# Optimization experiments

Hardware: AMD Instinct MI355X
Metric: run time of the kernel (lower is better)

## Reference

```python
import jax, jax.numpy as jnp
import numpy as np
import math

B, T, D, H, DFF = 4, 1024, 1024, 16, 4096
HD = D // H

def _c(a):
    # a: float array [2, ...] -> complex64 (a[0] real, a[1] imag)
    return jax.lax.complex(a[0], a[1])

def _clinear(z, W, b):
    # complex y = z @ W^T + b (torch nn.Linear convention)
    return z @ _c(W).T + _c(b)

def _cln(z, g, b, eps=1e-5):
    # per-component LayerNorm with separate affine for real/imag parts
    def ln(r):
        m = r.mean(-1, keepdims=True)
        v = ((r - m) ** 2).mean(-1, keepdims=True)
        return (r - m) / jnp.sqrt(v + eps)
    return jax.lax.complex(ln(z.real) * g[0] + b[0], ln(z.imag) * g[1] + b[1])

def _rope_phasor(t_len, dim):
    inv_freq = 1.0 / (10000.0 ** (jnp.arange(dim, dtype=jnp.float32) / dim))
    freqs = jnp.arange(t_len, dtype=jnp.float32)[:, None] * inv_freq[None, :]
    return jax.lax.complex(jnp.cos(freqs), jnp.sin(freqs))  # [T, HD]


def setup_inputs():
    key = jax.random.key(0)
    ks = iter(jax.random.split(key, 40))
    def p(shape, scale=0.02):
        return jax.random.normal(next(ks), shape, jnp.float32) * scale
    inp = {"x": p((2, B, T, D), 1.0), "mask": jnp.tril(jnp.ones((T, T), bool))}
    dims = {"wq": (D, D), "wk": (D, D), "wv": (D, D), "wo": (D, D),
            "wf1": (DFF, D), "wf2": (D, DFF), "wg": (D, D)}
    for name, (o, i) in dims.items():
        inp[name] = p((2, o, i))
        inp["b" + name[1:]] = p((2, o))
    inp["g1"] = jnp.ones((2, D), jnp.float32)
    inp["b1"] = jnp.zeros((2, D), jnp.float32)
    inp["g2"] = jnp.ones((2, D), jnp.float32)
    inp["b2"] = jnp.zeros((2, D), jnp.float32)
    return inp


def reference(x, mask, wq, bq, wk, bk, wv, bv, wo, bo,
              wf1, bf1, wf2, bf2, wg, bg, g1, b1, g2, b2):
    z = _c(x)  # [B,T,D] complex64
    ph = _rope_phasor(T, HD)[None, None]  # [1,1,T,HD]

    # ---- attention branch (pre-norm) ----
    nz = _cln(z, g1, b1)
    heads = lambda t: t.reshape(B, T, H, HD).transpose(0, 2, 1, 3)  # [B,H,T,HD]
    q = heads(_clinear(nz, wq, bq)) * ph
    k = heads(_clinear(nz, wk, bk)) * ph
    v = heads(_clinear(nz, wv, bv))
    score = jnp.einsum('bhqd,bhkd->bhqk', q, jnp.conj(k)) / math.sqrt(HD)
    mag = jnp.where(mask, jnp.abs(score), jnp.float32(-1e9))
    aw = jax.nn.softmax(mag, axis=-1)
    awc = jax.lax.complex(aw, jnp.zeros_like(aw))
    o = jnp.einsum('bhqk,bhkd->bhqd', awc, v)
    o = o.transpose(0, 2, 1, 3).reshape(B, T, D)
    z = z + _clinear(o, wo, bo)

    # ---- FFN branch with CReLU and AntiMatterGate ----
    nz = _cln(z, g2, b2)
    h = _clinear(nz, wf1, bf1)
    h = jax.lax.complex(jax.nn.relu(h.real), jax.nn.relu(h.imag))  # CReLU
    h = _clinear(h, wf2, bf2)
    g = _clinear(h, wg, bg)
    gn = jnp.abs(g) + 1e-8
    h = h * (g / jax.lax.complex(gn, jnp.zeros_like(gn)))  # phase-only gate
    z = z + h
    return jnp.stack([z.real, z.imag], axis=0)  # [2,B,T,D] float32
```

## Files before the change

kernel.cpp:

```cpp
#include <hip/hip_runtime.h>
#include <math.h>

#define B_ 4
#define T_ 1024
#define D_ 1024
#define H_ 16
#define DFF_ 4096
#define HD_ 64
#define BT_ (B_*T_)
#define PL ((size_t)BT_*D_)

typedef unsigned int uint;
typedef unsigned short ushort;
typedef __attribute__((ext_vector_type(8))) __bf16 bf16x8;
typedef __attribute__((ext_vector_type(4))) float f32x4;
typedef __attribute__((ext_vector_type(4))) uint uint4v;

__device__ __forceinline__ float b2f(ushort u){
  union{uint i; float f;} x; x.i = ((uint)u)<<16; return x.f;
}
__device__ __forceinline__ ushort f2b(float f){
  union{float f; uint i;} x; x.f = f;
  uint r = x.i + 0x7fffu + ((x.i>>16)&1u);
  return (ushort)(r>>16);
}
__device__ __forceinline__ void fsplit(float x, ushort& hi, ushort& lo){
  hi = f2b(x);
  lo = f2b(x - b2f(hi));
}
__device__ __forceinline__ bf16x8 negv(bf16x8 v){
  union{bf16x8 b; uint4v u;} t; t.b = v;
  t.u ^= 0x80008000u;
  return t.b;
}
__device__ __forceinline__ f32x4 mfma16(bf16x8 a, bf16x8 b, f32x4 c){
  return __builtin_amdgcn_mfma_f32_16x16x32_bf16(a,b,c,0,0,0);
}
__device__ __forceinline__ float block_sum(float v, float* sm){
  #pragma unroll
  for (int o=32;o>0;o>>=1) v += __shfl_down(v,o);
  int wid = threadIdx.x>>6;
  if ((threadIdx.x&63)==0) sm[wid]=v;
  __syncthreads();
  float r = sm[0]+sm[1]+sm[2]+sm[3];
  __syncthreads();
  return r;
}

__global__ __launch_bounds__(256) void cvt_split(const float* __restrict__ s,
                                                 ushort* __restrict__ d, long NK){
  long i = ((long)blockIdx.x*256 + threadIdx.x)*4;
  if (i >= NK) return;
  float4 vr = *(const float4*)(s+i);
  float4 vi = *(const float4*)(s+NK+i);
  ushort4 rh, rl, ih4, il4;
  fsplit(vr.x, rh.x, rl.x); fsplit(vr.y, rh.y, rl.y);
  fsplit(vr.z, rh.z, rl.z); fsplit(vr.w, rh.w, rl.w);
  fsplit(vi.x, ih4.x, il4.x); fsplit(vi.y, ih4.y, il4.y);
  fsplit(vi.z, ih4.z, il4.z); fsplit(vi.w, ih4.w, il4.w);
  *(ushort4*)(d + i)        = rh;
  *(ushort4*)(d + NK + i)   = rl;
  *(ushort4*)(d + 2*NK + i) = ih4;
  *(ushort4*)(d + 3*NK + i) = il4;
}

__global__ __launch_bounds__(256) void cln_kernel(const float* __restrict__ x,
    long PSx, int row0, const float* __restrict__ g, const float* __restrict__ bb,
    ushort* __restrict__ out, long PSo)
{
  __shared__ float sm[4];
  int row = blockIdx.x, comp = blockIdx.y;
  const float* xr = x + (size_t)comp*PSx + (size_t)(row0+row)*D_;
  float4 v = *(const float4*)(xr + threadIdx.x*4);
  float s = v.x+v.y+v.z+v.w;
  s = block_sum(s, sm);
  float mean = s * (1.0f/D_);
  float dx=v.x-mean, dy=v.y-mean, dz=v.z-mean, dw=v.w-mean;
  float s2 = dx*dx+dy*dy+dz*dz+dw*dw;
  s2 = block_sum(s2, sm);
  float inv = 1.0f/sqrtf(s2*(1.0f/D_) + 1e-5f);
  float4 gv = *(const float4*)(g + comp*D_ + threadIdx.x*4);
  float4 bv = *(const float4*)(bb + comp*D_ + threadIdx.x*4);
  float y0 = dx*inv*gv.x + bv.x, y1 = dy*inv*gv.y + bv.y;
  float y2 = dz*inv*gv.z + bv.z, y3 = dw*inv*gv.w + bv.w;
  ushort4 hh, ll;
  fsplit(y0, hh.x, ll.x); fsplit(y1, hh.y, ll.y);
  fsplit(y2, hh.z, ll.z); fsplit(y3, hh.w, ll.w);
  ushort* oh = out + (size_t)(comp*2)*PSo   + (size_t)row*D_;
  ushort* ol = out + (size_t)(comp*2+1)*PSo + (size_t)row*D_;
  *(ushort4*)(oh + threadIdx.x*4) = hh;
  *(ushort4*)(ol + threadIdx.x*4) = ll;
}

template<int BM,int BN,int WM,int WN>
__global__ __launch_bounds__(256,1) void cgemm_split(
    const ushort* __restrict__ A, long PSa,
    const ushort* __restrict__ W, long PSw, long wstride,
    const float* b0, const float* b1, const float* b2,
    const float* __restrict__ Rr, const float* __restrict__ Ri,
    float* __restrict__ Cf, long PSc, long ostrideF,
    ushort* __restrict__ Cs, long PSs, long ostrideS,
    int M, int N, int K, int relu, int biasRow, int kslice)
{
  constexpr int NI = WM/16, NJ = WN/16;
  constexpr int NWX = BN/WN;
  constexpr int NPW = (BM+BN)/16;
  constexpr int BUF = (BM+BN)*128;
  __shared__ __align__(16) ushort lds[2*BUF];
  const int tid = threadIdx.x, wave = tid>>6, lane = tid&63;
  const int quad = lane>>4, l16 = lane&15;
  const int lrow = lane>>3, sl = lane&7;

  const int gx = gridDim.x, gy = gridDim.y;
  const int nt = gx*gy;
  int lin = blockIdx.x + gx*blockIdx.y;
  int tile = (nt&7) ? lin : ((lin&7)*(nt>>3) + (lin>>3));
  int bxi, byi;
  if (gx <= gy){ bxi = tile % gx; byi = tile / gx; }
  else         { byi = tile % gy; bxi = tile / gy; }
  const int bm = byi*BM, bn = bxi*BN;

  const int gz = blockIdx.z;
  W += (size_t)gz*wstride;
  const float* bias = (gz==0)? b0 : (gz==1)? b1 : b2;
  if (Cf) Cf += (size_t)gz*ostrideF;
  if (Cs) Cs += (size_t)gz*ostrideS;
  const int wm = (wave/NWX)*WM, wn = (wave%NWX)*WN;
  const int kbeg = kslice ? gz*kslice : 0;
  const int kend = kslice ? kbeg+kslice : K;

  int sa[4];
  #pragma unroll
  for (int p=0;p<4;p++) sa[p] = (((p&1)<<2) + quad) ^ (l16&7);

  auto STAGE = [&](int cur, int k0){
    #pragma unroll
    for (int n=0;n<NPW;n++){
      int it = wave*NPW + n;
      const ushort* mat; long PS; int brow, pair, r0, lbase;
      if (it < BM/4){
        pair = it/(BM/8); r0 = (it%(BM/8))*8;
        mat = A; PS = PSa; brow = bm;
        lbase = (pair*BM + r0)*8;
      } else {
        int itb = it - BM/4;
        pair = itb/(BN/8); r0 = (itb%(BN/8))*8;
        mat = W; PS = PSw; brow = bn;
        lbase = (2*BM + pair*BN + r0)*8;
      }
      int row = r0 + lrow;
      int s = sl ^ (row&7);
      int plane = pair*2 + (s>>2);
      const ushort* gp = mat + (size_t)plane*PS + (size_t)(brow+row)*K + k0 + (s&3)*8;
      __builtin_amdgcn_global_load_lds(
          (const __attribute__((address_space(1))) void*)gp,
          (__attribute__((address_space(3))) void*)&lds[cur*BUF + lbase*8], 16, 0, 0);
    }
  };

  f32x4 accr[NI][NJ], acci[NI][NJ];
  #pragma unroll
  for (int i=0;i<NI;i++)
    #pragma unroll
    for (int j=0;j<NJ;j++){
      accr[i][j] = (f32x4){0.f,0.f,0.f,0.f};
      acci[i][j] = (f32x4){0.f,0.f,0.f,0.f};
    }

  int cur = 0;
  STAGE(0, kbeg);
  for (int k0=kbeg; k0<kend; k0+=32){
    __syncthreads();
    if (k0+32 < kend) STAGE(cur^1, k0+32);
    const int cb = cur*BUF;

    bf16x8 Bf[NJ][4];
    #pragma unroll
    for (int j=0;j<NJ;j++){
      int row = wn + j*16 + l16;
      #pragma unroll
      for (int p=0;p<4;p++)
        Bf[j][p] = *(const bf16x8*)&lds[cb + BM*128 + ((p>>1)*BN + row)*64 + sa[p]*8];
    }
    #pragma unroll
    for (int i=0;i<NI;i++){
      int row = wm + i*16 + l16;
      bf16x8 A0 = *(const bf16x8*)&lds[cb + (0*BM + row)*64 + sa[0]*8];
      bf16x8 A1 = *(const bf16x8*)&lds[cb + (0*BM + row)*64 + sa[1]*8];
      bf16x8 A2 = *(const bf16x8*)&lds[cb + (1*BM + row)*64 + sa[2]*8];
      bf16x8 A3 = *(const bf16x8*)&lds[cb + (1*BM + row)*64 + sa[3]*8];
      bf16x8 n2 = negv(A2), n3 = negv(A3);
      #pragma unroll
      for (int j=0;j<NJ;j++){
        f32x4 cr = accr[i][j], ci = acci[i][j];
        cr = mfma16(A0, Bf[j][0], cr); cr = mfma16(A0, Bf[j][1], cr); cr = mfma16(A1, Bf[j][0], cr);
        cr = mfma16(n2, Bf[j][2], cr); cr = mfma16(n2, Bf[j][3], cr); cr = mfma16(n3, Bf[j][2], cr);
        ci = mfma16(A0, Bf[j][2], ci); ci = mfma16(A0, Bf[j][3], ci); ci = mfma16(A1, Bf[j][2], ci);
        ci = mfma16(A2, Bf[j][0], ci); ci = mfma16(A2, Bf[j][1], ci); ci = mfma16(A3, Bf[j][0], ci);
        accr[i][j] = cr; acci[i][j] = ci;
      }
    }
    cur ^= 1;
  }
  #pragma unroll
  for (int i=0;i<NI;i++){
    #pragma unroll
    for (int j=0;j<NJ;j++){
      #pragma unroll
      for (int rg=0;rg<4;rg++){
        int row = bm + wm + i*16 + quad*4 + rg;
        int col = bn + wn + j*16 + l16;
        float br = 0.f, bi2 = 0.f;
        if (bias){
          br  = biasRow ? bias[row]   : bias[col];
          bi2 = biasRow ? bias[M+row] : bias[N+col];
        }
        float cr = accr[i][j][rg] + br;
        float ci = acci[i][j][rg] + bi2;
        size_t o = (size_t)row*N + col;
        if (Rr){ cr += Rr[o]; ci += Ri[o]; }
        if (relu){ cr = fmaxf(cr,0.f); ci = fmaxf(ci,0.f); }
        if (Cf){ Cf[o] = cr; Cf[PSc + o] = ci; }
        if (Cs){
          ushort h0,l0,h1v,l1;
          fsplit(cr,h0,l0); fsplit(ci,h1v,l1);
          Cs[o] = h0; Cs[PSs+o] = l0; Cs[2*PSs+o] = h1v; Cs[3*PSs+o] = l1;
        }
      }
    }
  }
}

__global__ __launch_bounds__(256) void rope_table(float* __restrict__ tab){
  int i = blockIdx.x*256 + threadIdx.x;
  int d = i & 63, t = i >> 6;
  float invf = expf(-(float)d * (9.210340371976184f/64.0f));
  float th = (float)t * invf;
  float s, c;
  sincosf(th, &s, &c);
  tab[2*i] = c; tab[2*i+1] = s;
}

__global__ __launch_bounds__(256) void rope_split(ushort* __restrict__ Q,
    ushort* __restrict__ Kk, const float* __restrict__ tab, long PS)
{
  size_t idx = (size_t)blockIdx.x*256 + threadIdx.x;
  int d = (int)(idx & (HD_-1));
  int t = (int)((idx >> 10) & (T_-1));
  float2 cs = *(const float2*)(tab + 2*(t*HD_ + d));
  float c = cs.x, s = cs.y;
  {
    float qr = b2f(Q[idx])      + b2f(Q[PS+idx]);
    float qi = b2f(Q[2*PS+idx]) + b2f(Q[3*PS+idx]);
    float nr = qr*c - qi*s, ni = qr*s + qi*c;
    ushort h,l;
    fsplit(nr,h,l); Q[idx]=h;      Q[PS+idx]=l;
    fsplit(ni,h,l); Q[2*PS+idx]=h; Q[3*PS+idx]=l;
  }
  {
    float kr = b2f(Kk[idx])      + b2f(Kk[PS+idx]);
    float ki = b2f(Kk[2*PS+idx]) + b2f(Kk[3*PS+idx]);
    float nr = kr*c - ki*s, ni = kr*s + ki*c;
    ushort h,l;
    fsplit(nr,h,l); Kk[idx]=h;      Kk[PS+idx]=l;
    fsplit(ni,h,l); Kk[2*PS+idx]=h; Kk[3*PS+idx]=l;
  }
}

__global__ __launch_bounds__(256) void attn_mfma(
    const ushort* __restrict__ Qg, const ushort* __restrict__ Kg,
    const ushort* __restrict__ Vt, long PS,
    ushort* __restrict__ O, long PSo)
{
  __shared__ __align__(16) ushort lds[24576];
  const int tid = threadIdx.x;
  const int wave = tid>>6, lane = tid&63;
  const int quad = lane>>4, l16 = lane&15;
  const int bh = blockIdx.x, b = bh>>4, h = bh&15;
  const int y = blockIdx.y;
  const int qb = (y<8) ? (15-y) : (y-8);
  const int qt0 = qb*64;
  const int qg = qt0 + wave*16 + l16;
  const int Pbase = 19456 + wave*1280;

  bf16x8 Qf[4][2];
  {
    size_t row = (size_t)(b*T_ + qt0 + wave*16 + l16);
    #pragma unroll
    for (int p=0;p<4;p++)
      #pragma unroll
      for (int dk=0;dk<2;dk++)
        Qf[p][dk] = *(const bf16x8*)(Qg + (size_t)p*PS + row*D_ + h*HD_ + dk*32 + quad*8);
  }
  f32x4 Or[4], Oi[4];
  #pragma unroll
  for (int dt=0;dt<4;dt++){ Or[dt]=(f32x4){0,0,0,0}; Oi[dt]=(f32x4){0,0,0,0}; }
  float mreg = -1e30f, lreg = 0.f;
  const int ntiles = 2*qb + 2;

  for (int tI=0; tI<ntiles; tI++){
    const int kt = tI*32;
    __syncthreads();
    #pragma unroll
    for (int r=0;r<4;r++){
      int id = r*256 + tid;
      int p = id>>8, rem = id&255;
      int row = rem>>3, slk = rem&7;
      const ushort* src = Kg + (size_t)p*PS + (size_t)(b*T_ + kt + row)*D_ + h*HD_ + slk*8;
      *(uint4*)&lds[p*2304 + row*72 + slk*8] = *(const uint4*)src;
    }
    {
      const ushort* srcp = Vt + (size_t)wave*PS + (size_t)(b*T_ + kt);
      #pragma unroll
      for (int r=0;r<4;r++){
        int chunk = r*64 + lane;
        int dd = chunk>>2, kg = chunk&3;
        *(uint4*)&lds[9216 + wave*2560 + dd*40 + kg*8] =
            *(const uint4*)(srcp + (size_t)(h*HD_ + dd)*BT_ + kg*8);
      }
    }
    __syncthreads();

    f32x4 sr[2], si[2];
    sr[0]=(f32x4){0,0,0,0}; sr[1]=(f32x4){0,0,0,0};
    si[0]=(f32x4){0,0,0,0}; si[1]=(f32x4){0,0,0,0};
    #pragma unroll
    for (int s=0;s<2;s++){
      #pragma unroll
      for (int dk=0;dk<2;dk++){
        int ra = (s*16+l16)*72 + dk*32 + quad*8;
        bf16x8 Krh = *(const bf16x8*)&lds[ra];
        bf16x8 Krl = *(const bf16x8*)&lds[2304 + ra];
        bf16x8 Kih = *(const bf16x8*)&lds[4608 + ra];
        bf16x8 Kil = *(const bf16x8*)&lds[6912 + ra];
        bf16x8 nKih = negv(Kih), nKil = negv(Kil);
        f32x4 r = sr[s], im = si[s];
        r = mfma16(Krh, Qf[0][dk], r); r = mfma16(Krh, Qf[1][dk], r); r = mfma16(Krl, Qf[0][dk], r);
        r = mfma16(Kih, Qf[2][dk], r); r = mfma16(Kih, Qf[3][dk], r); r = mfma16(Kil, Qf[2][dk], r);
        im = mfma16(Krh,  Qf[2][dk], im); im = mfma16(Krh,  Qf[3][dk], im); im = mfma16(Krl,  Qf[2][dk], im);
        im = mfma16(nKih, Qf[0][dk], im); im = mfma16(nKih, Qf[1][dk], im); im = mfma16(nKil, Qf[0][dk], im);
        sr[s]=r; si[s]=im;
      }
    }

    float pv[2][4];
    float mx = -1e30f;
    #pragma unroll
    for (int s=0;s<2;s++)
      #pragma unroll
      for (int rg=0;rg<4;rg++){
        float xr = sr[s][rg], xi = si[s][rg];
        float m = sqrtf(xr*xr + xi*xi)*0.125f;
        int kloc = kt + s*16 + quad*4 + rg;
        if (kloc > qg) m = -1e30f;
        pv[s][rg] = m;
        mx = fmaxf(mx, m);
      }
    mx = fmaxf(mx, __shfl_xor(mx,16));
    mx = fmaxf(mx, __shfl_xor(mx,32));
    float mnew = fmaxf(mreg, mx);
    float afac = __expf(mreg - mnew);
    float ps = 0.f;
    #pragma unroll
    for (int s=0;s<2;s++)
      #pragma unroll
      for (int rg=0;rg<4;rg++){
        float e = __expf(pv[s][rg] - mnew);
        pv[s][rg] = e; ps += e;
      }
    ps += __shfl_xor(ps,16); ps += __shfl_xor(ps,32);
    lreg = lreg*afac + ps;
    mreg = mnew;

    #pragma unroll
    for (int s=0;s<2;s++)
      #pragma unroll
      for (int rg=0;rg<4;rg++){
        ushort hi,lo; fsplit(pv[s][rg],hi,lo);
        int off = Pbase + l16*40 + s*16 + quad*4 + rg;
        lds[off] = hi; lds[off+640] = lo;
      }

    float af[4];
    #pragma unroll
    for (int rg=0;rg<4;rg++) af[rg] = __shfl(afac, quad*4+rg);
    #pragma unroll
    for (int dt=0;dt<4;dt++)
      #pragma unroll
      for (int rg=0;rg<4;rg++){ Or[dt][rg]*=af[rg]; Oi[dt][rg]*=af[rg]; }

    bf16x8 Ph  = *(const bf16x8*)&lds[Pbase +       l16*40 + quad*8];
    bf16x8 Plo = *(const bf16x8*)&lds[Pbase + 640 + l16*40 + quad*8];
    #pragma unroll
    for (int dt=0;dt<4;dt++){
      int rv = (dt*16+l16)*40 + quad*8;
      bf16x8 Vrh = *(const bf16x8*)&lds[9216 + rv];
      bf16x8 Vrl = *(const bf16x8*)&lds[9216 + 2560 + rv];
      bf16x8 Vih = *(const bf16x8*)&lds[9216 + 5120 + rv];
      bf16x8 Vil = *(const bf16x8*)&lds[9216 + 7680 + rv];
      f32x4 o_r = Or[dt], o_i = Oi[dt];
      o_r = mfma16(Ph, Vrh, o_r); o_r = mfma16(Ph, Vrl, o_r); o_r = mfma16(Plo, Vrh, o_r);
      o_i = mfma16(Ph, Vih, o_i); o_i = mfma16(Ph, Vil, o_i); o_i = mfma16(Plo, Vih, o_i);
      Or[dt]=o_r; Oi[dt]=o_i;
    }
  }

  float li[4];
  #pragma unroll
  for (int rg=0;rg<4;rg++) li[rg] = 1.0f / __shfl(lreg, quad*4+rg);
  #pragma unroll
  for (int dt=0;dt<4;dt++)
    #pragma unroll
    for (int rg=0;rg<4;rg++){
      float tr = Or[dt][rg]*li[rg], ti = Oi[dt][rg]*li[rg];
      ushort h0,l0,h1,l1;
      fsplit(tr,h0,l0); fsplit(ti,h1,l1);
      int rowt = qt0 + wave*16 + quad*4 + rg;
      size_t o = (size_t)(b*T_ + rowt)*D_ + h*HD_ + dt*16 + l16;
      O[o] = h0; O[PSo+o] = l0; O[2*PSo+o] = h1; O[3*PSo+o] = l1;
    }
}

__global__ __launch_bounds__(256) void hsum_kernel(const float* __restrict__ p0,
    const float* __restrict__ p1, ushort* __restrict__ out)
{
  size_t idx = (size_t)blockIdx.x*256 + threadIdx.x;
  const size_t M1s = (size_t)1<<20;
  float hr = p0[idx] + p1[idx];
  float hi = p0[M1s+idx] + p1[M1s+idx];
  ushort h0,l0,h1,l1;
  fsplit(hr,h0,l0); fsplit(hi,h1,l1);
  out[idx] = h0; out[M1s+idx] = l0; out[2*M1s+idx] = h1; out[3*M1s+idx] = l1;
}

__global__ __launch_bounds__(256) void gate_kernel(
    const float* __restrict__ z, const ushort* __restrict__ hB,
    const float* __restrict__ gp0, const float* __restrict__ gp1,
    float* __restrict__ out, int off)
{
  size_t idx = (size_t)blockIdx.x*256 + threadIdx.x;
  const size_t M1 = (size_t)1<<20;
  float hr = b2f(hB[idx])      + b2f(hB[M1+idx]);
  float hi = b2f(hB[2*M1+idx]) + b2f(hB[3*M1+idx]);
  float gr = gp0[idx] + gp1[idx];
  float gi = gp0[M1+idx] + gp1[M1+idx];
  float gn = sqrtf(gr*gr + gi*gi) + 1e-8f;
  float pr = (hr*gr - hi*gi) / gn;
  float pi = (hr*gi + hi*gr) / gn;
  size_t zoff = (size_t)off + idx;
  out[zoff]    = z[zoff] + pr;
  out[PL+zoff] = z[PL+zoff] + pi;
}

extern "C" void kernel_launch(void* const* d_in, const int* in_sizes, int n_in,
                              void* d_out, int out_size, void* d_ws, size_t ws_size,
                              hipStream_t stream)
{
  const float* x  = (const float*)d_in[0];
  const float* wq = (const float*)d_in[2];
  const float* bq = (const float*)d_in[3];
  const float* wk = (const float*)d_in[4];
  const float* bk = (const float*)d_in[5];
  const float* wv = (const float*)d_in[6];
  const float* bv = (const float*)d_in[7];
  const float* wo = (const float*)d_in[8];
  const float* bo = (const float*)d_in[9];
  const float* wf1= (const float*)d_in[10];
  const float* bf1= (const float*)d_in[11];
  const float* wf2= (const float*)d_in[12];
  const float* bf2= (const float*)d_in[13];
  const float* wg = (const float*)d_in[14];
  const float* bg = (const float*)d_in[15];
  const float* g1 = (const float*)d_in[16];
  const float* b1 = (const float*)d_in[17];
  const float* g2 = (const float*)d_in[18];
  const float* b2 = (const float*)d_in[19];
  float* out = (float*)d_out;
  char* w8 = (char*)d_ws;
  const size_t MB = (size_t)1<<20;
  const long M1 = 1L<<20, M4 = 1L<<22;

  ushort* wqkvB = (ushort*)(w8);
  ushort* woB   = (ushort*)(w8 + 24*MB);
  ushort* nzB   = (ushort*)(w8 + 32*MB);
  ushort* qS    = (ushort*)(w8 + 64*MB);
  ushort* kS    = (ushort*)(w8 + 96*MB);
  ushort* vtS   = (ushort*)(w8 + 128*MB);
  float*  ropeT = (float*)(w8 + 32*MB);
  ushort* oBc   = (ushort*)(w8 + 32*MB);
  float*  z     = (float*)(w8 + 64*MB);
  ushort* wf2B  = (ushort*)(w8);
  ushort* h1c   = (ushort*)(w8 + 32*MB);
  ushort* wf1B  = (ushort*)(w8 + 96*MB);
  ushort* wgB   = (ushort*)(w8 + 128*MB);
  ushort* nz2c  = (ushort*)(w8 + 136*MB);
  float*  p0F   = (float*)(w8 + 136*MB);
  ushort* hBc   = (ushort*)(w8 + 144*MB);
  float*  p1F   = (float*)(w8 + 152*MB);

  dim3 blk(256);
  cvt_split<<<1024, blk, 0, stream>>>(wq, wqkvB,        M1);
  cvt_split<<<1024, blk, 0, stream>>>(wk, wqkvB + 4*M1, M1);
  cvt_split<<<1024, blk, 0, stream>>>(wv, wqkvB + 8*M1, M1);
  cvt_split<<<1024, blk, 0, stream>>>(wo, woB,          M1);
  cln_kernel<<<dim3(BT_,2), blk, 0, stream>>>(x, (long)PL, 0, g1, b1, nzB, M4);
  cgemm_split<128,128,64,64><<<dim3(8,32,2), blk, 0, stream>>>(
      nzB, M4, wqkvB, M1, 4*M1, bq, bk, nullptr,
      nullptr, nullptr, nullptr, 0, 0, qS, M4, 4*M4,
      4096, 1024, 1024, 0, 0, 0);
  cgemm_split<128,128,64,64><<<dim3(32,8,1), blk, 0, stream>>>(
      wqkvB + 8*M1, M1, nzB, M4, 0, bv, nullptr, nullptr,
      nullptr, nullptr, nullptr, 0, 0, vtS, M4, 0,
      1024, 4096, 1024, 0, 1, 0);
  rope_table<<<256, blk, 0, stream>>>(ropeT);
  rope_split<<<16384, blk, 0, stream>>>(qS, kS, ropeT, M4);
  attn_mfma<<<dim3(64,16), blk, 0, stream>>>(qS, kS, vtS, M4, oBc, M4);
  cgemm_split<128,128,64,64><<<dim3(8,32,1), blk, 0, stream>>>(
      oBc, M4, woB, M1, 0, bo, nullptr, nullptr,
      x, x + PL, z, (long)PL, 0, nullptr, 0, 0,
      4096, 1024, 1024, 0, 0, 0);
  cvt_split<<<4096, blk, 0, stream>>>(wf1, wf1B, M4);
  cvt_split<<<4096, blk, 0, stream>>>(wf2, wf2B, M4);
  cvt_split<<<1024, blk, 0, stream>>>(wg, wgB, M1);
  for (int c=0; c<4; c++){
    cln_kernel<<<dim3(1024,2), blk, 0, stream>>>(z, (long)PL, c*1024, g2, b2, nz2c, M1);
    cgemm_split<128,128,64,64><<<dim3(32,8,1), blk, 0, stream>>>(
        nz2c, M1, wf1B, M4, 0, bf1, nullptr, nullptr,
        nullptr, nullptr, nullptr, 0, 0, h1c, M4, 0,
        1024, 4096, 1024, 1, 0, 0);
    cgemm_split<128,64,64,32><<<dim3(16,8,2), blk, 0, stream>>>(
        h1c, M4, wf2B, M4, 0, bf2, nullptr, nullptr,
        nullptr, nullptr, p0F, M1, M4, nullptr, 0, 0,
        1024, 1024, 4096, 0, 0, 2048);
    hsum_kernel<<<4096, blk, 0, stream>>>(p0F, p1F, hBc);
    cgemm_split<128,64,64,32><<<dim3(16,8,2), blk, 0, stream>>>(
        hBc, M1, wgB, M1, 0, bg, nullptr, nullptr,
        nullptr, nullptr, p0F, M1, M4, nullptr, 0, 0,
        1024, 1024, 1024, 0, 0, 512);
    gate_kernel<<<4096, blk, 0, stream>>>(z, hBc, p0F, p1F, out, c*(int)M1);
  }
}
```

Measured before the change: 1.904 ms.

## Shrink GEMM tiles to 64x64, single-buffer LDS, and raise occupancy

Every complex GEMM now uses 64x64 block tiles with 32x32 warp tiles instead of 128x128/128x64 tiles. The LDS double buffer is replaced by a single buffer, with a second barrier after the loads, and global pointers are precomputed once and advanced each K step. Launch bounds now request three blocks per SM so latency is hidden by occupancy rather than prefetch. The risk is lower per-block data reuse, more global/L2 traffic, and serialized load-then-compute within each block.

```diff
diff --git a/kernel.cpp b/kernel.cpp
--- a/kernel.cpp
+++ b/kernel.cpp
@@ -92,8 +92,8 @@
   *(ushort4*)(ol + threadIdx.x*4) = ll;
 }
 
-template<int BM,int BN,int WM,int WN>
-__global__ __launch_bounds__(256,1) void cgemm_split(
+template<int BM,int BN,int WM,int WN,int NT>
+__global__ __launch_bounds__(NT,3) void cgemm_split(
     const ushort* __restrict__ A, long PSa,
     const ushort* __restrict__ W, long PSw, long wstride,
     const float* b0, const float* b1, const float* b2,
@@ -104,9 +104,8 @@
 {
   constexpr int NI = WM/16, NJ = WN/16;
   constexpr int NWX = BN/WN;
-  constexpr int NPW = (BM+BN)/16;
-  constexpr int BUF = (BM+BN)*128;
-  __shared__ __align__(16) ushort lds[2*BUF];
+  constexpr int NPW = (BM+BN)*16/NT;
+  __shared__ __align__(16) ushort lds[(BM+BN)*128];
   const int tid = threadIdx.x, wave = tid>>6, lane = tid&63;
   const int quad = lane>>4, l16 = lane&15;
   const int lrow = lane>>3, sl = lane&7;
@@ -133,30 +132,28 @@
   #pragma unroll
   for (int p=0;p<4;p++) sa[p] = (((p&1)<<2) + quad) ^ (l16&7);
 
-  auto STAGE = [&](int cur, int k0){
-    #pragma unroll
-    for (int n=0;n<NPW;n++){
-      int it = wave*NPW + n;
-      const ushort* mat; long PS; int brow, pair, r0, lbase;
-      if (it < BM/4){
-        pair = it/(BM/8); r0 = (it%(BM/8))*8;
-        mat = A; PS = PSa; brow = bm;
-        lbase = (pair*BM + r0)*8;
-      } else {
-        int itb = it - BM/4;
-        pair = itb/(BN/8); r0 = (itb%(BN/8))*8;
-        mat = W; PS = PSw; brow = bn;
-        lbase = (2*BM + pair*BN + r0)*8;
-      }
-      int row = r0 + lrow;
-      int s = sl ^ (row&7);
-      int plane = pair*2 + (s>>2);
-      const ushort* gp = mat + (size_t)plane*PS + (size_t)(brow+row)*K + k0 + (s&3)*8;
-      __builtin_amdgcn_global_load_lds(
-          (const __attribute__((address_space(1))) void*)gp,
-          (__attribute__((address_space(3))) void*)&lds[cur*BUF + lbase*8], 16, 0, 0);
-    }
-  };
+  const ushort* gp[NPW];
+  int lofs[NPW];
+  #pragma unroll
+  for (int n=0;n<NPW;n++){
+    int it = wave*NPW + n;
+    const ushort* mat; long PS; int brow, pair, r0, lbase;
+    if (it < BM/4){
+      pair = it/(BM/8); r0 = (it%(BM/8))*8;
+      mat = A; PS = PSa; brow = bm;
+      lbase = (pair*BM + r0)*8;
+    } else {
+      int itb = it - BM/4;
+      pair = itb/(BN/8); r0 = (itb%(BN/8))*8;
+      mat = W; PS = PSw; brow = bn;
+      lbase = (2*BM + pair*BN + r0)*8;
+    }
+    int row = r0 + lrow;
+    int s = sl ^ (row&7);
+    int plane = pair*2 + (s>>2);
+    gp[n] = mat + (size_t)plane*PS + (size_t)(brow+row)*K + kbeg + (s&3)*8;
+    lofs[n] = lbase*8;
+  }
 
   f32x4 accr[NI][NJ], acci[NI][NJ];
   #pragma unroll
@@ -167,12 +164,16 @@
       acci[i][j] = (f32x4){0.f,0.f,0.f,0.f};
     }
 
-  int cur = 0;
-  STAGE(0, kbeg);
   for (int k0=kbeg; k0<kend; k0+=32){
     __syncthreads();
-    if (k0+32 < kend) STAGE(cur^1, k0+32);
-    const int cb = cur*BUF;
+    #pragma unroll
+    for (int n=0;n<NPW;n++){
+      __builtin_amdgcn_global_load_lds(
+          (const __attribute__((address_space(1))) void*)gp[n],
+          (__attribute__((address_space(3))) void*)&lds[lofs[n]], 16, 0, 0);
+      gp[n] += 32;
+    }
+    __syncthreads();
 
     bf16x8 Bf[NJ][4];
     #pragma unroll
@@ -180,15 +181,15 @@
       int row = wn + j*16 + l16;
       #pragma unroll
       for (int p=0;p<4;p++)
-        Bf[j][p] = *(const bf16x8*)&lds[cb + BM*128 + ((p>>1)*BN + row)*64 + sa[p]*8];
+        Bf[j][p] = *(const bf16x8*)&lds[BM*128 + ((p>>1)*BN + row)*64 + sa[p]*8];
     }
     #pragma unroll
     for (int i=0;i<NI;i++){
       int row = wm + i*16 + l16;
-      bf16x8 A0 = *(const bf16x8*)&lds[cb + (0*BM + row)*64 + sa[0]*8];
-      bf16x8 A1 = *(const bf16x8*)&lds[cb + (0*BM + row)*64 + sa[1]*8];
-      bf16x8 A2 = *(const bf16x8*)&lds[cb + (1*BM + row)*64 + sa[2]*8];
-      bf16x8 A3 = *(const bf16x8*)&lds[cb + (1*BM + row)*64 + sa[3]*8];
+      bf16x8 A0 = *(const bf16x8*)&lds[(0*BM + row)*64 + sa[0]*8];
+      bf16x8 A1 = *(const bf16x8*)&lds[(0*BM + row)*64 + sa[1]*8];
+      bf16x8 A2 = *(const bf16x8*)&lds[(1*BM + row)*64 + sa[2]*8];
+      bf16x8 A3 = *(const bf16x8*)&lds[(1*BM + row)*64 + sa[3]*8];
       bf16x8 n2 = negv(A2), n3 = negv(A3);
       #pragma unroll
       for (int j=0;j<NJ;j++){
@@ -200,7 +201,6 @@
         accr[i][j] = cr; acci[i][j] = ci;
       }
     }
-    cur ^= 1;
   }
   #pragma unroll
   for (int i=0;i<NI;i++){
@@ -504,18 +504,18 @@
   cvt_split<<<1024, blk, 0, stream>>>(wv, wqkvB + 8*M1, M1);
   cvt_split<<<1024, blk, 0, stream>>>(wo, woB,          M1);
   cln_kernel<<<dim3(BT_,2), blk, 0, stream>>>(x, (long)PL, 0, g1, b1, nzB, M4);
-  cgemm_split<128,128,64,64><<<dim3(8,32,2), blk, 0, stream>>>(
+  cgemm_split<64,64,32,32,256><<<dim3(16,64,2), blk, 0, stream>>>(
       nzB, M4, wqkvB, M1, 4*M1, bq, bk, nullptr,
       nullptr, nullptr, nullptr, 0, 0, qS, M4, 4*M4,
       4096, 1024, 1024, 0, 0, 0);
-  cgemm_split<128,128,64,64><<<dim3(32,8,1), blk, 0, stream>>>(
+  cgemm_split<64,64,32,32,256><<<dim3(64,16,1), blk, 0, stream>>>(
       wqkvB + 8*M1, M1, nzB, M4, 0, bv, nullptr, nullptr,
       nullptr, nullptr, nullptr, 0, 0, vtS, M4, 0,
       1024, 4096, 1024, 0, 1, 0);
   rope_table<<<256, blk, 0, stream>>>(ropeT);
   rope_split<<<16384, blk, 0, stream>>>(qS, kS, ropeT, M4);
   attn_mfma<<<dim3(64,16), blk, 0, stream>>>(qS, kS, vtS, M4, oBc, M4);
-  cgemm_split<128,128,64,64><<<dim3(8,32,1), blk, 0, stream>>>(
+  cgemm_split<64,64,32,32,256><<<dim3(16,64,1), blk, 0, stream>>>(
       oBc, M4, woB, M1, 0, bo, nullptr, nullptr,
       x, x + PL, z, (long)PL, 0, nullptr, 0, 0,
       4096, 1024, 1024, 0, 0, 0);
@@ -524,16 +524,16 @@
   cvt_split<<<1024, blk, 0, stream>>>(wg, wgB, M1);
   for (int c=0; c<4; c++){
     cln_kernel<<<dim3(1024,2), blk, 0, stream>>>(z, (long)PL, c*1024, g2, b2, nz2c, M1);
-    cgemm_split<128,128,64,64><<<dim3(32,8,1), blk, 0, stream>>>(
+    cgemm_split<64,64,32,32,256><<<dim3(64,16,1), blk, 0, stream>>>(
         nz2c, M1, wf1B, M4, 0, bf1, nullptr, nullptr,
         nullptr, nullptr, nullptr, 0, 0, h1c, M4, 0,
         1024, 4096, 1024, 1, 0, 0);
-    cgemm_split<128,64,64,32><<<dim3(16,8,2), blk, 0, stream>>>(
+    cgemm_split<64,64,32,32,256><<<dim3(16,16,2), blk, 0, stream>>>(
         h1c, M4, wf2B, M4, 0, bf2, nullptr, nullptr,
         nullptr, nullptr, p0F, M1, M4, nullptr, 0, 0,
         1024, 1024, 4096, 0, 0, 2048);
     hsum_kernel<<<4096, blk, 0, stream>>>(p0F, p1F, hBc);
-    cgemm_split<128,64,64,32><<<dim3(16,8,2), blk, 0, stream>>>(
+    cgemm_split<64,64,32,32,256><<<dim3(16,16,2), blk, 0, stream>>>(
         hBc, M1, wgB, M1, 0, bg, nullptr, nullptr,
         nullptr, nullptr, p0F, M1, M4, nullptr, 0, 0,
         1024, 1024, 1024, 0, 0, 512);
```

Result: faster. 1.802 ms (-5.4%).
